# Kernel optimization log

Hardware: AMD Instinct MI355X
Metric: run time of the kernel (lower is better)

## Reference

```python
import jax, jax.numpy as jnp
import numpy as np

NUM_CLASSES = 32
SIGMA = 0.02
LOG_SIGMA = float(np.log(SIGMA))
HALF_LOG_2PI = float(0.5 * np.log(2.0 * np.pi))


def _gcn(x, adj, W1, b1, W2, b2):
    # Two-layer GCN: h = relu(A x W1 + b1); out = A h W2 + b2
    h = jax.nn.relu(jnp.einsum('bij,bjf->bif', adj, x) @ W1 + b1)
    return jnp.einsum('bij,bjf->bif', adj, h) @ W2 + b2


def setup_inputs() -> dict:
    key = jax.random.key(0)
    ks = jax.random.split(key, 10)
    B, N, F = 64, 1024, 512
    x = jax.random.normal(ks[0], (B, N, F), dtype=jnp.float32)
    adj = jax.random.uniform(ks[1], (B, N, N), dtype=jnp.float32) / N  # row-scaled dense adjacency
    masks = jax.random.randint(ks[2], (B, N, F), 0, 2, dtype=jnp.int32)
    noise = jax.random.normal(ks[3], (B, N, F), dtype=jnp.float32)
    s = 0.05
    We1 = jax.random.normal(ks[4], (F, 30), dtype=jnp.float32) * s
    be1 = jnp.zeros((30,), dtype=jnp.float32)
    We2 = jax.random.normal(ks[5], (30, 18), dtype=jnp.float32) * s
    be2 = jnp.zeros((18,), dtype=jnp.float32)
    Wd1 = jax.random.normal(ks[6], (18, 30), dtype=jnp.float32) * s
    bd1 = jnp.zeros((30,), dtype=jnp.float32)
    Wd2 = jax.random.normal(ks[7], (30, F), dtype=jnp.float32) * s
    bd2 = jnp.zeros((F,), dtype=jnp.float32)
    return dict(x=x, adj=adj, masks=masks, noise=noise, We1=We1, be1=be1,
                We2=We2, be2=be2, Wd1=Wd1, bd1=bd1, Wd2=Wd2, bd2=bd2)


def reference(x, adj, masks, noise, We1, be1, We2, be2, Wd1, bd1, Wd2, bd2):
    enc = _gcn(x, adj, We1, be1, We2, be2)            # [B,N,18]
    dec = _gcn(enc, adj, Wd1, bd1, Wd2, bd2)          # [B,N,F]
    dec_act = jnp.concatenate(
        (jax.nn.softmax(dec[..., :NUM_CLASSES], axis=-1),
         jax.nn.sigmoid(dec[..., NUM_CLASSES:])), axis=-1)
    m = masks.astype(dec_act.dtype)
    # Vectorized masked reparameterized Gaussian sample: s = mu + sigma*eps
    sampled = dec_act + m * (SIGMA * noise)
    # log N(s; mu, sigma) = -eps^2/2 - log(sigma) - 0.5*log(2pi), summed over masked entries
    lp_elem = -0.5 * noise * noise - LOG_SIGMA - HALF_LOG_2PI
    log_probs = jnp.sum(m * lp_elem, axis=(1, 2))      # [B]
    return dec, sampled, log_probs
```

## Files before the change

kernel.cpp:

```cpp
#include <hip/hip_runtime.h>

#define B_ 64
#define NN 1024
#define FF 512

typedef float  fx4 __attribute__((ext_vector_type(4)));
typedef int    ix4 __attribute__((ext_vector_type(4)));
typedef unsigned int   ux4i __attribute__((ext_vector_type(4)));
typedef unsigned short us4  __attribute__((ext_vector_type(4)));
typedef short  sx8 __attribute__((ext_vector_type(8)));

static __device__ __forceinline__ unsigned short f2bf(float f){
    union { float f; unsigned u; } v; v.f = f;
    unsigned r = v.u + 0x7FFFu + ((v.u >> 16) & 1u);
    return (unsigned short)(r >> 16);
}
static __device__ __forceinline__ float bf2f(unsigned short h){
    union { unsigned u; float f; } v; v.u = ((unsigned)h) << 16;
    return v.f;
}

__global__ __launch_bounds__(512) void k_xw1(
    const float* __restrict__ x, const float* __restrict__ We1,
    unsigned short* __restrict__ u1T){
    __shared__ unsigned short wls[32*512];
    int tid = threadIdx.x;
    for (int i = tid; i < 32*512; i += 512){
        int col = i >> 9, k = i & 511;
        float v = (col < 30) ? We1[k*30 + col] : 0.f;
        wls[col*512 + ((((k >> 3) ^ (col & 7)) << 3) | (k & 7))] = f2bf(v);
    }
    __syncthreads();
    int w = tid >> 6, l = tid & 63;
    int lr = l & 15, kq = l >> 4;
    int b = blockIdx.y;
    int rowb = blockIdx.x*128 + w*16;
    const float* xp = x + ((size_t)b*NN + rowb + lr)*FF + kq*8;
    fx4 acc0 = {0,0,0,0}, acc1 = {0,0,0,0};
    int c0 = lr, c1 = 16 + lr;
    #pragma unroll 4
    for (int kk = 0; kk < FF; kk += 32){
        fx4 v0 = *(const fx4*)(xp + kk);
        fx4 v1 = *(const fx4*)(xp + kk + 4);
        sx8 a;
        #pragma unroll
        for (int t = 0; t < 4; t++){ a[t] = (short)f2bf(v0[t]); a[4+t] = (short)f2bf(v1[t]); }
        int chunk = (kk >> 3) + kq;
        sx8 b0 = *(const sx8*)(wls + c0*512 + ((chunk ^ (c0 & 7)) << 3));
        sx8 b1 = *(const sx8*)(wls + c1*512 + ((chunk ^ (c1 & 7)) << 3));
        acc0 = __builtin_amdgcn_mfma_f32_16x16x32_bf16(a, b0, acc0, 0, 0, 0);
        acc1 = __builtin_amdgcn_mfma_f32_16x16x32_bf16(a, b1, acc1, 0, 0, 0);
    }
    int row0 = rowb + kq*4;
    us4 o0 = { f2bf(acc0[0]), f2bf(acc0[1]), f2bf(acc0[2]), f2bf(acc0[3]) };
    us4 o1 = { f2bf(acc1[0]), f2bf(acc1[1]), f2bf(acc1[2]), f2bf(acc1[3]) };
    *(us4*)(u1T + ((size_t)b*32 + c0)*NN + row0) = o0;
    *(us4*)(u1T + ((size_t)b*32 + c1)*NN + row0) = o1;
}

template<int CVT, int RM>
__global__ __launch_bounds__(256) void k_adjmm(
    const float* __restrict__ adjf,
    const unsigned short* __restrict__ adjb_in,
    unsigned short* __restrict__ adjb_out,
    const unsigned short* __restrict__ uT,
    const float* __restrict__ bias, int biasN, int relu,
    unsigned short* __restrict__ outT){
    __shared__ unsigned short uts[32*NN];
    int tid = threadIdx.x;
    int rt = blockIdx.x, b = blockIdx.y;
    const ux4i* src = (const ux4i*)(uT + (size_t)b*32*NN);
    #pragma unroll
    for (int i = 0; i < 16; i++){
        int j = tid + i*256;
        int c = j >> 7;
        ux4i v = src[j];
        int dst = (j*16) ^ ((c & 7) << 4);
        *(ux4i*)((char*)uts + dst) = v;
    }
    __syncthreads();
    int w = tid >> 6, l = tid & 63;
    int lr = l & 15, lk = (l >> 4) * 8;
    size_t aoff = (size_t)b*NN*NN + (size_t)(rt*128 + w*32 + lr)*NN + lk;
    int c0 = lr, c1 = 16 + lr;
    fx4 acc00 = {0,0,0,0}, acc01 = {0,0,0,0}, acc10 = {0,0,0,0}, acc11 = {0,0,0,0};
    #pragma unroll 4
    for (int kk = 0; kk < NN; kk += 32){
        sx8 a0, a1;
        if (CVT){
            fx4 v00 = *(const fx4*)(adjf + aoff + kk);
            fx4 v01 = *(const fx4*)(adjf + aoff + kk + 4);
            fx4 v10 = *(const fx4*)(adjf + aoff + 16*NN + kk);
            fx4 v11 = *(const fx4*)(adjf + aoff + 16*NN + kk + 4);
            #pragma unroll
            for (int t = 0; t < 4; t++){
                a0[t] = (short)f2bf(v00[t]); a0[4+t] = (short)f2bf(v01[t]);
                a1[t] = (short)f2bf(v10[t]); a1[4+t] = (short)f2bf(v11[t]);
            }
            *(sx8*)(adjb_out + aoff + kk) = a0;
            *(sx8*)(adjb_out + aoff + 16*NN + kk) = a1;
        } else {
            a0 = *(const sx8*)(adjb_in + aoff + kk);
            a1 = *(const sx8*)(adjb_in + aoff + 16*NN + kk);
        }
        int kb = (kk + lk) * 2;
        sx8 b0 = *(const sx8*)((const char*)uts + ((c0*2048 + kb) ^ ((c0 & 7) << 4)));
        sx8 b1 = *(const sx8*)((const char*)uts + ((c1*2048 + kb) ^ ((c1 & 7) << 4)));
        acc00 = __builtin_amdgcn_mfma_f32_16x16x32_bf16(a0, b0, acc00, 0, 0, 0);
        acc01 = __builtin_amdgcn_mfma_f32_16x16x32_bf16(a0, b1, acc01, 0, 0, 0);
        acc10 = __builtin_amdgcn_mfma_f32_16x16x32_bf16(a1, b0, acc10, 0, 0, 0);
        acc11 = __builtin_amdgcn_mfma_f32_16x16x32_bf16(a1, b1, acc11, 0, 0, 0);
    }
    float bias0 = 0.f, bias1 = 0.f;
    if (bias){
        if (c0 < biasN) bias0 = bias[c0];
        if (c1 < biasN) bias1 = bias[c1];
    }
    int lq = l >> 4;
    #pragma unroll
    for (int mt = 0; mt < 2; mt++){
        int row0 = rt*128 + w*32 + mt*16 + lq*4;
        fx4 am0 = mt ? acc10 : acc00;
        fx4 am1 = mt ? acc11 : acc01;
        #pragma unroll
        for (int ct = 0; ct < 2; ct++){
            fx4 a = ct ? am1 : am0;
            float bb = ct ? bias1 : bias0;
            int col = ct ? c1 : c0;
            us4 o;
            #pragma unroll
            for (int j = 0; j < 4; j++){
                float v = a[j] + bb;
                if (relu) v = fmaxf(v, 0.f);
                o[j] = f2bf(v);
            }
            if (RM){
                #pragma unroll
                for (int j = 0; j < 4; j++)
                    outT[((size_t)b*NN + row0 + j)*32 + col] = o[j];
            } else {
                *(us4*)(outT + ((size_t)b*32 + col)*NN + row0) = o;
            }
        }
    }
}

template<int JI, int CO, bool RELU>
__global__ __launch_bounds__(256) void k_tiny(
    const unsigned short* __restrict__ inT, const float* __restrict__ W,
    const float* __restrict__ bias, unsigned short* __restrict__ outT){
    int n = blockIdx.x*256 + threadIdx.x;
    int b = blockIdx.y;
    const unsigned short* ip = inT + (size_t)b*32*NN + n;
    float in[JI];
    #pragma unroll
    for (int j = 0; j < JI; j++) in[j] = bf2f(ip[j*NN]);
    float acc[CO];
    #pragma unroll
    for (int c = 0; c < CO; c++) acc[c] = bias ? bias[c] : 0.f;
    #pragma unroll
    for (int j = 0; j < JI; j++){
        #pragma unroll
        for (int c = 0; c < CO; c++) acc[c] += in[j] * W[j*CO + c];
    }
    unsigned short* op = outT + (size_t)b*32*NN + n;
    #pragma unroll
    for (int c = 0; c < 32; c++){
        float v = (c < CO) ? (RELU ? fmaxf(acc[c], 0.f) : acc[c]) : 0.f;
        op[c*NN] = f2bf(v);
    }
}

__global__ __launch_bounds__(512, 4) void k_dec(
    const unsigned short* __restrict__ v2R,
    const float* __restrict__ Wd2, const float* __restrict__ bd2,
    const int* __restrict__ masks, const float* __restrict__ noise,
    float* __restrict__ dec, float* __restrict__ sampled, float* __restrict__ part){
    __shared__ unsigned short wls[512*40];
    __shared__ float dls[16][516];
    __shared__ float red[8];
    int tid = threadIdx.x;
    for (int i = tid; i < 512*32; i += 512){
        int col = i & 511, k = i >> 9;
        float v = (k < 30) ? Wd2[k*512 + col] : 0.f;
        wls[col*40 + k] = f2bf(v);
    }
    int w = tid >> 6, l = tid & 63;
    int lr = l & 15, kq = l >> 4;
    const float LPC = 2.9930844722234733f;
    float lpacc = 0.f;
    __syncthreads();
    #pragma unroll
    for (int it = 0; it < 4; it++){
        int rbase = blockIdx.x*64 + it*16;
        sx8 a = *(const sx8*)(v2R + (size_t)(rbase + lr)*32 + kq*8);
        #pragma unroll
        for (int i = 0; i < 4; i++){
            int c = (w + 8*i)*16 + lr;
            sx8 bb = *(const sx8*)(wls + c*40 + kq*8);
            fx4 acc = {0,0,0,0};
            acc = __builtin_amdgcn_mfma_f32_16x16x32_bf16(a, bb, acc, 0, 0, 0);
            float bi = bd2[c];
            #pragma unroll
            for (int j = 0; j < 4; j++)
                dls[kq*4 + j][c] = acc[j] + bi;
        }
        __syncthreads();
        #pragma unroll
        for (int s = 0; s < 2; s++){
            int rloc = w + 8*s;
            size_t off = (size_t)(rbase + rloc)*FF + l*8;
            fx4 d0 = *(const fx4*)&dls[rloc][l*8];
            fx4 d1 = *(const fx4*)&dls[rloc][l*8 + 4];
            ix4 m0 = *(const ix4*)(masks + off);
            ix4 m1 = *(const ix4*)(masks + off + 4);
            fx4 z0 = *(const fx4*)(noise + off);
            fx4 z1 = *(const fx4*)(noise + off + 4);
            float av[8];
            #pragma unroll
            for (int i = 0; i < 4; i++){
                av[i]   = 1.f/(1.f + __expf(-d0[i]));
                av[4+i] = 1.f/(1.f + __expf(-d1[i]));
            }
            if (l < 4){
                float mx = d0[0];
                #pragma unroll
                for (int i = 1; i < 4; i++) mx = fmaxf(mx, d0[i]);
                #pragma unroll
                for (int i = 0; i < 4; i++) mx = fmaxf(mx, d1[i]);
                mx = fmaxf(mx, __shfl_xor(mx, 1, 4));
                mx = fmaxf(mx, __shfl_xor(mx, 2, 4));
                float e[8], ss = 0.f;
                #pragma unroll
                for (int i = 0; i < 4; i++){ e[i] = __expf(d0[i] - mx); ss += e[i]; }
                #pragma unroll
                for (int i = 0; i < 4; i++){ e[4+i] = __expf(d1[i] - mx); ss += e[4+i]; }
                ss += __shfl_xor(ss, 1, 4);
                ss += __shfl_xor(ss, 2, 4);
                float inv = 1.f / ss;
                #pragma unroll
                for (int i = 0; i < 8; i++) av[i] = e[i]*inv;
            }
            *(fx4*)(dec + off)     = d0;
            *(fx4*)(dec + off + 4) = d1;
            fx4 sm0, sm1;
            #pragma unroll
            for (int i = 0; i < 4; i++){
                float mi0 = (float)m0[i], zi0 = z0[i];
                float mi1 = (float)m1[i], zi1 = z1[i];
                sm0[i] = av[i]   + mi0*(0.02f*zi0);
                sm1[i] = av[4+i] + mi1*(0.02f*zi1);
                lpacc = fmaf(mi0, LPC - 0.5f*zi0*zi0, lpacc);
                lpacc = fmaf(mi1, LPC - 0.5f*zi1*zi1, lpacc);
            }
            *(fx4*)(sampled + off)     = sm0;
            *(fx4*)(sampled + off + 4) = sm1;
        }
        __syncthreads();
    }
    #pragma unroll
    for (int off = 32; off > 0; off >>= 1) lpacc += __shfl_xor(lpacc, off);
    if (l == 0) red[w] = lpacc;
    __syncthreads();
    if (tid == 0){
        float s = 0.f;
        #pragma unroll
        for (int i = 0; i < 8; i++) s += red[i];
        part[blockIdx.x] = s;
    }
}

__global__ void k_lp(const float* __restrict__ part, float* __restrict__ logp){
    int t = threadIdx.x;
    float s = 0.f;
    #pragma unroll
    for (int i = 0; i < 16; i++) s += part[t*16 + i];
    logp[t] = s;
}

extern "C" void kernel_launch(void* const* d_in, const int* in_sizes, int n_in,
                              void* d_out, int out_size, void* d_ws, size_t ws_size,
                              hipStream_t stream){
    const float* x     = (const float*)d_in[0];
    const float* adj   = (const float*)d_in[1];
    const int*   masks = (const int*)  d_in[2];
    const float* noise = (const float*)d_in[3];
    const float* We1   = (const float*)d_in[4];
    const float* be1   = (const float*)d_in[5];
    const float* We2   = (const float*)d_in[6];
    const float* be2   = (const float*)d_in[7];
    const float* Wd1   = (const float*)d_in[8];
    const float* bd1   = (const float*)d_in[9];
    const float* Wd2   = (const float*)d_in[10];
    const float* bd2   = (const float*)d_in[11];

    float* dec     = (float*)d_out;
    float* sampled = dec + (size_t)B_*NN*FF;
    float* logp    = sampled + (size_t)B_*NN*FF;
    unsigned short* adjb = (unsigned short*)d_out;
    unsigned short* bufA = (unsigned short*)d_ws;
    unsigned short* bufB = bufA + (size_t)B_*32*NN;
    float* part = (float*)bufB;

    k_xw1<<<dim3(8, B_), 512, 0, stream>>>(x, We1, bufA);
    k_adjmm<1,0><<<dim3(8, B_), 256, 0, stream>>>(adj, nullptr, adjb, bufA, be1, 30, 1, bufB);
    k_tiny<30,18,false><<<dim3(4, B_), 256, 0, stream>>>(bufB, We2, nullptr, bufA);
    k_adjmm<0,0><<<dim3(8, B_), 256, 0, stream>>>(nullptr, adjb, nullptr, bufA, be2, 18, 0, bufB);
    k_adjmm<0,0><<<dim3(8, B_), 256, 0, stream>>>(nullptr, adjb, nullptr, bufB, nullptr, 0, 0, bufA);
    k_tiny<18,30,true><<<dim3(4, B_), 256, 0, stream>>>(bufA, Wd1, bd1, bufB);
    k_adjmm<0,1><<<dim3(8, B_), 256, 0, stream>>>(nullptr, adjb, nullptr, bufB, nullptr, 0, 0, bufA);
    k_dec<<<1024, 512, 0, stream>>>(bufA, Wd2, bd2, masks, noise, dec, sampled, part);
    k_lp<<<1, 64, 0, stream>>>(part, logp);
}
```

Before: 377.3 us.

## Store scaled adjacency copy as fp8 to halve reread traffic

The first adjacency pass now writes a scaled FP8 (x16384) copy of adj instead of a bf16 copy. The later four adjacency matmuls read these 1-byte values, unpack them to bf16 for the MFMA, and fold the inverse scale into the bias epilogues and the tiny-layer outputs. The aim is to halve the memory traffic of the repeated 64x1024x1024 adjacency reads, which dominate the bandwidth. In exchange it adds conversion ALU work per element and a real loss of precision in adj, since uniform values around 1e-3 are quantized to fp8.

```diff
diff --git a/kernel.cpp b/kernel.cpp
--- a/kernel.cpp
+++ b/kernel.cpp
@@ -5,10 +5,15 @@
 #define FF 512
 
 typedef float  fx4 __attribute__((ext_vector_type(4)));
+typedef float  fx2 __attribute__((ext_vector_type(2)));
 typedef int    ix4 __attribute__((ext_vector_type(4)));
 typedef unsigned int   ux4i __attribute__((ext_vector_type(4)));
+typedef unsigned int   ux2i __attribute__((ext_vector_type(2)));
 typedef unsigned short us4  __attribute__((ext_vector_type(4)));
 typedef short  sx8 __attribute__((ext_vector_type(8)));
+
+#define FP8_SCALE   16384.0f
+#define INV_SCALE   6.103515625e-5f
 
 static __device__ __forceinline__ unsigned short f2bf(float f){
     union { float f; unsigned u; } v; v.f = f;
@@ -58,13 +63,9 @@
     *(us4*)(u1T + ((size_t)b*32 + c1)*NN + row0) = o1;
 }
 
-template<int CVT, int RM>
-__global__ __launch_bounds__(256) void k_adjmm(
-    const float* __restrict__ adjf,
-    const unsigned short* __restrict__ adjb_in,
-    unsigned short* __restrict__ adjb_out,
-    const unsigned short* __restrict__ uT,
-    const float* __restrict__ bias, int biasN, int relu,
+__global__ __launch_bounds__(256) void k_cvt_h1(
+    const float* __restrict__ adjf, unsigned char* __restrict__ adj8,
+    const unsigned short* __restrict__ uT, const float* __restrict__ bias,
     unsigned short* __restrict__ outT){
     __shared__ unsigned short uts[32*NN];
     int tid = threadIdx.x;
@@ -86,22 +87,30 @@
     fx4 acc00 = {0,0,0,0}, acc01 = {0,0,0,0}, acc10 = {0,0,0,0}, acc11 = {0,0,0,0};
     #pragma unroll 4
     for (int kk = 0; kk < NN; kk += 32){
+        fx4 v00 = *(const fx4*)(adjf + aoff + kk);
+        fx4 v01 = *(const fx4*)(adjf + aoff + kk + 4);
+        fx4 v10 = *(const fx4*)(adjf + aoff + 16*NN + kk);
+        fx4 v11 = *(const fx4*)(adjf + aoff + 16*NN + kk + 4);
         sx8 a0, a1;
-        if (CVT){
-            fx4 v00 = *(const fx4*)(adjf + aoff + kk);
-            fx4 v01 = *(const fx4*)(adjf + aoff + kk + 4);
-            fx4 v10 = *(const fx4*)(adjf + aoff + 16*NN + kk);
-            fx4 v11 = *(const fx4*)(adjf + aoff + 16*NN + kk + 4);
-            #pragma unroll
-            for (int t = 0; t < 4; t++){
-                a0[t] = (short)f2bf(v00[t]); a0[4+t] = (short)f2bf(v01[t]);
-                a1[t] = (short)f2bf(v10[t]); a1[4+t] = (short)f2bf(v11[t]);
-            }
-            *(sx8*)(adjb_out + aoff + kk) = a0;
-            *(sx8*)(adjb_out + aoff + 16*NN + kk) = a1;
-        } else {
-            a0 = *(const sx8*)(adjb_in + aoff + kk);
-            a1 = *(const sx8*)(adjb_in + aoff + 16*NN + kk);
+        #pragma unroll
+        for (int t = 0; t < 4; t++){
+            a0[t] = (short)f2bf(v00[t]); a0[4+t] = (short)f2bf(v01[t]);
+            a1[t] = (short)f2bf(v10[t]); a1[4+t] = (short)f2bf(v11[t]);
+        }
+        {
+            const float S = FP8_SCALE;
+            int d0 = __builtin_amdgcn_cvt_pk_fp8_f32(v00[0]*S, v00[1]*S, 0, false);
+            d0     = __builtin_amdgcn_cvt_pk_fp8_f32(v00[2]*S, v00[3]*S, d0, true);
+            int d1 = __builtin_amdgcn_cvt_pk_fp8_f32(v01[0]*S, v01[1]*S, 0, false);
+            d1     = __builtin_amdgcn_cvt_pk_fp8_f32(v01[2]*S, v01[3]*S, d1, true);
+            ux2i s0 = { (unsigned)d0, (unsigned)d1 };
+            *(ux2i*)(adj8 + aoff + kk) = s0;
+            int d2 = __builtin_amdgcn_cvt_pk_fp8_f32(v10[0]*S, v10[1]*S, 0, false);
+            d2     = __builtin_amdgcn_cvt_pk_fp8_f32(v10[2]*S, v10[3]*S, d2, true);
+            int d3 = __builtin_amdgcn_cvt_pk_fp8_f32(v11[0]*S, v11[1]*S, 0, false);
+            d3     = __builtin_amdgcn_cvt_pk_fp8_f32(v11[2]*S, v11[3]*S, d3, true);
+            ux2i s1 = { (unsigned)d2, (unsigned)d3 };
+            *(ux2i*)(adj8 + aoff + 16*NN + kk) = s1;
         }
         int kb = (kk + lk) * 2;
         sx8 b0 = *(const sx8*)((const char*)uts + ((c0*2048 + kb) ^ ((c0 & 7) << 4)));
@@ -111,11 +120,9 @@
         acc10 = __builtin_amdgcn_mfma_f32_16x16x32_bf16(a1, b0, acc10, 0, 0, 0);
         acc11 = __builtin_amdgcn_mfma_f32_16x16x32_bf16(a1, b1, acc11, 0, 0, 0);
     }
-    float bias0 = 0.f, bias1 = 0.f;
-    if (bias){
-        if (c0 < biasN) bias0 = bias[c0];
-        if (c1 < biasN) bias1 = bias[c1];
-    }
+    float bias0 = (c0 < 30) ? bias[c0] : 0.f;
+    float bias1 = 0.f;
+    if (c1 < 30) bias1 = bias[c1];
     int lq = l >> 4;
     #pragma unroll
     for (int mt = 0; mt < 2; mt++){
@@ -130,8 +137,87 @@
             us4 o;
             #pragma unroll
             for (int j = 0; j < 4; j++){
-                float v = a[j] + bb;
-                if (relu) v = fmaxf(v, 0.f);
+                float v = fmaxf(a[j] + bb, 0.f);
+                o[j] = f2bf(v);
+            }
+            *(us4*)(outT + ((size_t)b*32 + col)*NN + row0) = o;
+        }
+    }
+}
+
+template<int RM>
+__global__ __launch_bounds__(256) void k_adjf8(
+    const unsigned char* __restrict__ adj8,
+    const unsigned short* __restrict__ uT,
+    const float* __restrict__ bias, int biasN, float oscale,
+    unsigned short* __restrict__ outT){
+    __shared__ unsigned short uts[32*NN];
+    int tid = threadIdx.x;
+    int rt = blockIdx.x, b = blockIdx.y;
+    const ux4i* src = (const ux4i*)(uT + (size_t)b*32*NN);
+    #pragma unroll
+    for (int i = 0; i < 16; i++){
+        int j = tid + i*256;
+        int c = j >> 7;
+        ux4i v = src[j];
+        int dst = (j*16) ^ ((c & 7) << 4);
+        *(ux4i*)((char*)uts + dst) = v;
+    }
+    __syncthreads();
+    int w = tid >> 6, l = tid & 63;
+    int lr = l & 15, lk = (l >> 4) * 8;
+    size_t aoff = (size_t)b*NN*NN + (size_t)(rt*128 + w*32 + lr)*NN + lk;
+    int c0 = lr, c1 = 16 + lr;
+    fx4 acc00 = {0,0,0,0}, acc01 = {0,0,0,0}, acc10 = {0,0,0,0}, acc11 = {0,0,0,0};
+    #pragma unroll 4
+    for (int kk = 0; kk < NN; kk += 32){
+        ux2i q0 = *(const ux2i*)(adj8 + aoff + kk);
+        ux2i q1 = *(const ux2i*)(adj8 + aoff + 16*NN + kk);
+        fx2 f0 = __builtin_amdgcn_cvt_pk_f32_fp8((int)q0[0], false);
+        fx2 f1 = __builtin_amdgcn_cvt_pk_f32_fp8((int)q0[0], true);
+        fx2 f2 = __builtin_amdgcn_cvt_pk_f32_fp8((int)q0[1], false);
+        fx2 f3 = __builtin_amdgcn_cvt_pk_f32_fp8((int)q0[1], true);
+        fx2 g0 = __builtin_amdgcn_cvt_pk_f32_fp8((int)q1[0], false);
+        fx2 g1 = __builtin_amdgcn_cvt_pk_f32_fp8((int)q1[0], true);
+        fx2 g2 = __builtin_amdgcn_cvt_pk_f32_fp8((int)q1[1], false);
+        fx2 g3 = __builtin_amdgcn_cvt_pk_f32_fp8((int)q1[1], true);
+        sx8 a0, a1;
+        a0[0]=(short)f2bf(f0[0]); a0[1]=(short)f2bf(f0[1]);
+        a0[2]=(short)f2bf(f1[0]); a0[3]=(short)f2bf(f1[1]);
+        a0[4]=(short)f2bf(f2[0]); a0[5]=(short)f2bf(f2[1]);
+        a0[6]=(short)f2bf(f3[0]); a0[7]=(short)f2bf(f3[1]);
+        a1[0]=(short)f2bf(g0[0]); a1[1]=(short)f2bf(g0[1]);
+        a1[2]=(short)f2bf(g1[0]); a1[3]=(short)f2bf(g1[1]);
+        a1[4]=(short)f2bf(g2[0]); a1[5]=(short)f2bf(g2[1]);
+        a1[6]=(short)f2bf(g3[0]); a1[7]=(short)f2bf(g3[1]);
+        int kb = (kk + lk) * 2;
+        sx8 b0 = *(const sx8*)((const char*)uts + ((c0*2048 + kb) ^ ((c0 & 7) << 4)));
+        sx8 b1 = *(const sx8*)((const char*)uts + ((c1*2048 + kb) ^ ((c1 & 7) << 4)));
+        acc00 = __builtin_amdgcn_mfma_f32_16x16x32_bf16(a0, b0, acc00, 0, 0, 0);
+        acc01 = __builtin_amdgcn_mfma_f32_16x16x32_bf16(a0, b1, acc01, 0, 0, 0);
+        acc10 = __builtin_amdgcn_mfma_f32_16x16x32_bf16(a1, b0, acc10, 0, 0, 0);
+        acc11 = __builtin_amdgcn_mfma_f32_16x16x32_bf16(a1, b1, acc11, 0, 0, 0);
+    }
+    float bias0 = 0.f, bias1 = 0.f;
+    if (bias){
+        if (c0 < biasN) bias0 = bias[c0];
+        if (c1 < biasN) bias1 = bias[c1];
+    }
+    int lq = l >> 4;
+    #pragma unroll
+    for (int mt = 0; mt < 2; mt++){
+        int row0 = rt*128 + w*32 + mt*16 + lq*4;
+        fx4 am0 = mt ? acc10 : acc00;
+        fx4 am1 = mt ? acc11 : acc01;
+        #pragma unroll
+        for (int ct = 0; ct < 2; ct++){
+            fx4 a = ct ? am1 : am0;
+            float bb = ct ? bias1 : bias0;
+            int col = ct ? c1 : c0;
+            us4 o;
+            #pragma unroll
+            for (int j = 0; j < 4; j++){
+                float v = (a[j] + bb) * oscale;
                 o[j] = f2bf(v);
             }
             if (RM){
@@ -148,7 +234,8 @@
 template<int JI, int CO, bool RELU>
 __global__ __launch_bounds__(256) void k_tiny(
     const unsigned short* __restrict__ inT, const float* __restrict__ W,
-    const float* __restrict__ bias, unsigned short* __restrict__ outT){
+    const float* __restrict__ bias, float oscale,
+    unsigned short* __restrict__ outT){
     int n = blockIdx.x*256 + threadIdx.x;
     int b = blockIdx.y;
     const unsigned short* ip = inT + (size_t)b*32*NN + n;
@@ -166,7 +253,7 @@
     unsigned short* op = outT + (size_t)b*32*NN + n;
     #pragma unroll
     for (int c = 0; c < 32; c++){
-        float v = (c < CO) ? (RELU ? fmaxf(acc[c], 0.f) : acc[c]) : 0.f;
+        float v = (c < CO) ? (RELU ? fmaxf(acc[c], 0.f) : acc[c]) * oscale : 0.f;
         op[c*NN] = f2bf(v);
     }
 }
@@ -297,18 +384,18 @@
     float* dec     = (float*)d_out;
     float* sampled = dec + (size_t)B_*NN*FF;
     float* logp    = sampled + (size_t)B_*NN*FF;
-    unsigned short* adjb = (unsigned short*)d_out;
+    unsigned char* adj8 = (unsigned char*)d_out;
     unsigned short* bufA = (unsigned short*)d_ws;
     unsigned short* bufB = bufA + (size_t)B_*32*NN;
     float* part = (float*)bufB;
 
     k_xw1<<<dim3(8, B_), 512, 0, stream>>>(x, We1, bufA);
-    k_adjmm<1,0><<<dim3(8, B_), 256, 0, stream>>>(adj, nullptr, adjb, bufA, be1, 30, 1, bufB);
-    k_tiny<30,18,false><<<dim3(4, B_), 256, 0, stream>>>(bufB, We2, nullptr, bufA);
-    k_adjmm<0,0><<<dim3(8, B_), 256, 0, stream>>>(nullptr, adjb, nullptr, bufA, be2, 18, 0, bufB);
-    k_adjmm<0,0><<<dim3(8, B_), 256, 0, stream>>>(nullptr, adjb, nullptr, bufB, nullptr, 0, 0, bufA);
-    k_tiny<18,30,true><<<dim3(4, B_), 256, 0, stream>>>(bufA, Wd1, bd1, bufB);
-    k_adjmm<0,1><<<dim3(8, B_), 256, 0, stream>>>(nullptr, adjb, nullptr, bufB, nullptr, 0, 0, bufA);
+    k_cvt_h1<<<dim3(8, B_), 256, 0, stream>>>(adj, adj8, bufA, be1, bufB);
+    k_tiny<30,18,false><<<dim3(4, B_), 256, 0, stream>>>(bufB, We2, nullptr, INV_SCALE, bufA);
+    k_adjf8<0><<<dim3(8, B_), 256, 0, stream>>>(adj8, bufA, be2, 18, INV_SCALE, bufB);
+    k_adjf8<0><<<dim3(8, B_), 256, 0, stream>>>(adj8, bufB, nullptr, 0, 1.0f, bufA);
+    k_tiny<18,30,true><<<dim3(4, B_), 256, 0, stream>>>(bufA, Wd1, bd1, INV_SCALE, bufB);
+    k_adjf8<1><<<dim3(8, B_), 256, 0, stream>>>(adj8, bufB, nullptr, 0, 1.0f, bufA);
     k_dec<<<1024, 512, 0, stream>>>(bufA, Wd2, bd2, masks, noise, dec, sampled, part);
     k_lp<<<1, 64, 0, stream>>>(part, logp);
 }
```

Measured after the change: 349.9 us. 7.3% less time.
